# Kernel optimization log

Measured on AMD Instinct MI355X. Metric: run time of the kernel, lower is better.

Reference implementation:

```python
import jax, jax.numpy as jnp
import numpy as np

D = 128            # actual_dim
DM = 2 * D         # d_model = 256
DI = 2 * DM        # support-encoder inner dim = 512
H = 2 * DM         # LSTMCell hidden = 512
NUM_SYMBOLS = 200000
KNN_K = 10
PROCESS_STEPS = 4
BQ, BS, NN = 4096, 128, 64


def setup_inputs() -> dict:
    key = jax.random.key(0)
    ks = jax.random.split(key, 20)
    ri = lambda k, shape, hi: jax.random.randint(k, shape, 0, hi)
    rn = lambda k, shape, s=0.05: jax.random.normal(k, shape, jnp.float32) * s
    emb = rn(ks[0], (NUM_SYMBOLS + 1, D), 0.1).at[NUM_SYMBOLS].set(0.0)  # padding row
    return {
        "query": ri(ks[1], (BQ, 2), NUM_SYMBOLS),
        "support": ri(ks[2], (BS, 2), NUM_SYMBOLS),
        "q_l_conn": ri(ks[3], (BQ, NN, 2), NUM_SYMBOLS),
        "q_l_deg": ri(ks[4], (BQ,), NN),
        "q_r_conn": ri(ks[5], (BQ, NN, 2), NUM_SYMBOLS),
        "q_r_deg": ri(ks[6], (BQ,), NN),
        "s_l_conn": ri(ks[7], (BS, NN, 2), NUM_SYMBOLS),
        "s_l_deg": ri(ks[8], (BS,), NN),
        "s_r_conn": ri(ks[9], (BS, NN, 2), NUM_SYMBOLS),
        "s_r_deg": ri(ks[10], (BS,), NN),
        "emb": emb,
        "gcn_W": rn(ks[11], (D, 2 * D)),
        "gcn_wb": jnp.zeros((D,), jnp.float32),
        "gcn_b": jnp.zeros((D,), jnp.float32),
        "se_w1": rn(ks[12], (DI, DM)),
        "se_b1": jnp.zeros((DI,), jnp.float32),
        "se_w2": rn(ks[13], (DM, DI)),
        "se_b2": jnp.zeros((DM,), jnp.float32),
        "ln_g": jnp.ones((DM,), jnp.float32),
        "ln_b": jnp.zeros((DM,), jnp.float32),
        "W_ih": rn(ks[14], (4 * H, DM)),
        "W_hh": rn(ks[15], (4 * H, H)),
        "b_ih": jnp.zeros((4 * H,), jnp.float32),
        "b_hh": jnp.zeros((4 * H,), jnp.float32),
    }


def _cos(a, b, eps=1e-8):
    num = jnp.sum(a * b, -1)
    den = jnp.maximum(jnp.linalg.norm(a, axis=-1), eps) * jnp.maximum(jnp.linalg.norm(b, axis=-1), eps)
    return num / den


def _neighbor_encoder(emb, gcn_W, gcn_wb, gcn_b, conn, ent_ids):
    rel = emb[conn[..., 0]]                     # [B,N,D]
    ent = emb[conn[..., 1]]                     # [B,N,D]
    center = emb[ent_ids][:, None, :]           # [B,1,D]
    sim = _cos(center, ent)                     # [B,N]
    _, idx = jax.lax.top_k(sim, KNN_K)          # [B,K]
    rel_k = jnp.take_along_axis(rel, idx[..., None], axis=1)
    ent_k = jnp.take_along_axis(ent, idx[..., None], axis=1)
    cat = jnp.concatenate([rel_k, ent_k], -1)   # [B,K,2D]
    h = jnp.einsum('bkf,df->bkd', cat, gcn_W) + gcn_wb + gcn_b
    return jnp.tanh(h.mean(axis=1))             # [B,D]


def _support_encoder(x, w1, b1, w2, b2, g, b):
    # residual FFN + LayerNorm (GMatching SupportEncoder), dropout off (eval)
    out = jax.nn.relu(x @ w1.T + b1) @ w2.T + b2
    y = out + x
    mu = y.mean(-1, keepdims=True)
    var = ((y - mu) ** 2).mean(-1, keepdims=True)
    return (y - mu) / jnp.sqrt(var + 1e-5) * g + b


def _query_encoder(support, query, W_ih, W_hh, b_ih, b_hh):
    # GMatching attentive LSTM process block. support: [1,DM], query: [B,DM]
    B = query.shape[0]
    h_r = jnp.zeros((B, H), query.dtype)
    c = jnp.zeros((B, H), query.dtype)
    h = query
    for _ in range(PROCESS_STEPS):
        gates = query @ W_ih.T + b_ih + h_r @ W_hh.T + b_hh
        i, f, g_, o = jnp.split(gates, 4, axis=-1)  # torch LSTMCell gate order
        c = jax.nn.sigmoid(f) * c + jax.nn.sigmoid(i) * jnp.tanh(g_)
        h_new = jax.nn.sigmoid(o) * jnp.tanh(c)     # [B,H]
        h = query + h_new[:, :DM]                   # [B,DM]
        attn = jax.nn.softmax(h @ support.T, axis=1)  # [B,1]
        r = attn @ support                          # [B,DM]
        h_r = jnp.concatenate([h, r], axis=1)       # [B,H]
    return h


def reference(query, support, q_l_conn, q_l_deg, q_r_conn, q_r_deg,
              s_l_conn, s_l_deg, s_r_conn, s_r_deg,
              emb, gcn_W, gcn_wb, gcn_b,
              se_w1, se_b1, se_w2, se_b2, ln_g, ln_b,
              W_ih, W_hh, b_ih, b_hh):
    ne = lambda conn, ids: _neighbor_encoder(emb, gcn_W, gcn_wb, gcn_b, conn, ids)
    q_nb = jnp.concatenate([ne(q_l_conn, query[:, 0]), ne(q_r_conn, query[:, 1])], -1)    # [BQ,DM]
    s_nb = jnp.concatenate([ne(s_l_conn, support[:, 0]), ne(s_r_conn, support[:, 1])], -1)  # [BS,DM]
    se = lambda x: _support_encoder(x, se_w1, se_b1, se_w2, se_b2, ln_g, ln_b)
    support_g = se(s_nb).mean(axis=0, keepdims=True)  # [1,DM]
    query_g = se(q_nb)                                # [BQ,DM]
    qf = _query_encoder(support_g, query_g, W_ih, W_hh, b_ih, b_hh)
    l2 = lambda x: x / jnp.maximum(jnp.linalg.norm(x, axis=-1, keepdims=True), 1e-12)
    return (l2(qf) @ l2(support_g).T).squeeze(-1)     # [BQ]
```

## Files before the change

kernel.cpp:

```cpp
#include <hip/hip_runtime.h>
#include <hip/hip_bf16.h>

#define D   128
#define DM  256
#define DI  512
#define HH  512
#define KNN 10
#define NN  64
#define BQ  4096
#define BS  128
#define BM2 (BQ + BS)
#define G2  1024
#define GK  256
#define NSYM 200000
#define NEB (BQ * 2 + BS * 2)
#define BKT 64
#define LDP (BKT + 8)

__device__ __forceinline__ float sigmoidf_(float x) {
    return 1.f / (1.f + __expf(-x));
}
__device__ __forceinline__ float tanh_fast(float x) {
    x = fminf(fmaxf(x, -20.f), 20.f);
    float e = __expf(2.f * x);
    return (e - 1.f) / (e + 1.f);
}
__device__ __forceinline__ ushort f2bf(float x) {
    union { float f; unsigned u; } v; v.f = x;
    unsigned r = (v.u + 0x7fffu + ((v.u >> 16) & 1u)) >> 16;
    return (ushort)r;
}

typedef __bf16  bf16x8  __attribute__((ext_vector_type(8)));
typedef float   floatx4 __attribute__((ext_vector_type(4)));

__global__ __launch_bounds__(256) void ne_prep_kernel(
    const int* __restrict__ q_l, const int* __restrict__ q_r,
    const int* __restrict__ q_ids,
    const int* __restrict__ s_l, const int* __restrict__ s_r,
    const int* __restrict__ s_ids,
    const float* __restrict__ emb,
    float* __restrict__ catm_out,
    const float* __restrict__ W_ih, const float* __restrict__ W_hh,
    const float* __restrict__ b_ih, const float* __restrict__ b_hh,
    const float* __restrict__ se_w1, const float* __restrict__ se_w2,
    ushort* __restrict__ wih_bf, ushort* __restrict__ whh_bf,
    float* __restrict__ bsumP, ushort* __restrict__ w1_bf,
    ushort* __restrict__ w2_bf)
{
    int bid = blockIdx.x;
    int tid = threadIdx.x;

    if (bid >= NEB) {
        int pb = bid - NEB;
        if (pb < G2) {
            int n = pb;
            int bn = n >> 7, r = n & 127;
            int half = (r >> 6) & 1, j = (r >> 4) & 3, l = r & 15;
            int u = bn * 32 + half * 16 + l;
            int oldrow = j * 512 + u;
            wih_bf[n * 256 + tid] = f2bf(W_ih[(size_t)oldrow * DM + tid]);
            whh_bf[n * 256 + tid] = f2bf(W_hh[(size_t)oldrow * HH + tid]);
            if (tid == 0) bsumP[n] = b_ih[oldrow] + b_hh[oldrow];
        } else {
            int idx = (pb - G2) * 256 + tid;
            w1_bf[idx] = f2bf(se_w1[idx]);
            w2_bf[idx] = f2bf(se_w2[idx]);
        }
        return;
    }

    const int *conn_l, *conn_r, *ids;
    int row;
    if (bid < BQ * 2) { conn_l = q_l; conn_r = q_r; ids = q_ids; row = bid >> 1; }
    else { conn_l = s_l; conn_r = s_r; ids = s_ids; row = (bid - BQ * 2) >> 1; }
    int side = bid & 1;
    const int* conn = (side ? conn_r : conn_l) + (size_t)row * NN * 2;
    int cid = ids[row * 2 + side];

    __shared__ int   connb[NN * 2];
    __shared__ float sim[NN];
    __shared__ int   selr[KNN], sele[KNN];

    int wave = tid >> 6, lane = tid & 63;
    int grp = lane >> 4, l16 = lane & 15;

    if (tid < NN * 2) connb[tid] = conn[tid];
    const float* cp = &emb[(size_t)cid * D + l16 * 8];
    float4 c4a = *(const float4*)cp;
    float4 c4b = *(const float4*)(cp + 4);
    float cs = c4a.x * c4a.x + c4a.y * c4a.y + c4a.z * c4a.z + c4a.w * c4a.w
             + c4b.x * c4b.x + c4b.y * c4b.y + c4b.z * c4b.z + c4b.w * c4b.w;
    #pragma unroll
    for (int off = 8; off; off >>= 1) cs += __shfl_xor(cs, off);
    float cnorm = fmaxf(sqrtf(cs), 1e-8f);
    __syncthreads();

    float4 ea[4], eb[4];
    #pragma unroll
    for (int b = 0; b < 4; b++) {
        int j = wave * 16 + b * 4 + grp;
        int eid = connb[j * 2 + 1];
        const float* ep = &emb[(size_t)eid * D + l16 * 8];
        ea[b] = *(const float4*)ep;
        eb[b] = *(const float4*)(ep + 4);
    }
    #pragma unroll
    for (int b = 0; b < 4; b++) {
        int j = wave * 16 + b * 4 + grp;
        float dot = c4a.x * ea[b].x + c4a.y * ea[b].y + c4a.z * ea[b].z + c4a.w * ea[b].w
                  + c4b.x * eb[b].x + c4b.y * eb[b].y + c4b.z * eb[b].z + c4b.w * eb[b].w;
        float ee  = ea[b].x * ea[b].x + ea[b].y * ea[b].y + ea[b].z * ea[b].z + ea[b].w * ea[b].w
                  + eb[b].x * eb[b].x + eb[b].y * eb[b].y + eb[b].z * eb[b].z + eb[b].w * eb[b].w;
        #pragma unroll
        for (int off = 8; off; off >>= 1) {
            dot += __shfl_xor(dot, off);
            ee  += __shfl_xor(ee, off);
        }
        if (l16 == 0) sim[j] = dot / (cnorm * fmaxf(sqrtf(ee), 1e-8f));
    }
    __syncthreads();

    if (wave == 0) {
        float s = sim[lane];
        int id = lane;
        for (int k = 0; k < KNN; k++) {
            float bs = s; int bi = id;
            #pragma unroll
            for (int off = 32; off; off >>= 1) {
                float os = __shfl_xor(bs, off);
                int   oi = __shfl_xor(bi, off);
                if (os > bs || (os == bs && oi < bi)) { bs = os; bi = oi; }
            }
            if (lane == 0) { selr[k] = connb[bi * 2]; sele[k] = connb[bi * 2 + 1]; }
            if (id == bi) s = -__builtin_inff();
        }
    }
    __syncthreads();

    float acc = 0.f;
    if (tid < D) {
        #pragma unroll
        for (int k = 0; k < KNN; k++) acc += emb[(size_t)selr[k] * D + tid];
    } else {
        int d = tid - D;
        #pragma unroll
        for (int k = 0; k < KNN; k++) acc += emb[(size_t)sele[k] * D + d];
    }
    catm_out[(size_t)bid * DM + tid] = acc * (1.f / KNN);
}

#define GR 16
__global__ __launch_bounds__(256) void gcn_kernel(
    const float* __restrict__ catm, const float* __restrict__ gcn_W,
    const float* __restrict__ gcn_wb, const float* __restrict__ gcn_b,
    float* __restrict__ out, ushort* __restrict__ out_bf)
{
    __shared__ float cs[GR][DM];
    __shared__ float pp[GR][DM];
    int tid = threadIdx.x;
    int m0 = blockIdx.x * GR;
    #pragma unroll
    for (int t = 0; t < 4; t++) {
        int chunk = tid + 256 * t;
        int r = chunk >> 6, c4 = chunk & 63;
        *(float4*)&cs[r][c4 * 4] = *(const float4*)&catm[(size_t)(m0 + r) * DM + c4 * 4];
    }
    __syncthreads();

    int d = tid & 127, half = tid >> 7;
    float a[GR];
    #pragma unroll
    for (int r = 0; r < GR; r++) a[r] = 0.f;
    const float4* W4 = (const float4*)(gcn_W + (size_t)d * DM + half * D);
    for (int f4 = 0; f4 < D / 4; ++f4) {
        float4 w = W4[f4];
        #pragma unroll
        for (int r = 0; r < GR; r++) {
            const float* c = &cs[r][half * D + f4 * 4];
            a[r] += w.x * c[0] + w.y * c[1] + w.z * c[2] + w.w * c[3];
        }
    }
    #pragma unroll
    for (int r = 0; r < GR; r++) pp[r][tid] = a[r];
    __syncthreads();
    if (tid < D) {
        #pragma unroll
        for (int r = 0; r < GR; r++) {
            float h = pp[r][tid] + pp[r][tid + D] + gcn_wb[tid] + gcn_b[tid];
            float th = tanh_fast(h);
            out[(size_t)(m0 + r) * D + tid] = th;
            out_bf[(size_t)(m0 + r) * D + tid] = f2bf(th);
        }
    }
}

#define GEMM64_VARS()                                                         \
    __shared__ __align__(16) ushort As[64][LDP];                              \
    __shared__ __align__(16) ushort Bs[128][LDP];                             \
    int tid = threadIdx.x;                                                    \
    int wave = tid >> 6, lane = tid & 63;                                     \
    int quad = lane >> 4, l16 = lane & 15;                                    \
    int wm = (wave >> 1) * 32, wn = (wave & 1) * 64;

#define GEMM64_CORE(AP, BP, KDIM)                                             \
    floatx4 acc[2][4];                                                        \
    _Pragma("unroll")                                                         \
    for (int i = 0; i < 2; i++)                                               \
        _Pragma("unroll")                                                     \
        for (int j = 0; j < 4; j++) acc[i][j] = (floatx4){0.f, 0.f, 0.f, 0.f};\
    for (int k0 = 0; k0 < (KDIM); k0 += BKT) {                                \
        __syncthreads();                                                      \
        _Pragma("unroll")                                                     \
        for (int t = 0; t < 2; t++) {                                         \
            int ch = t * 256 + tid;                                           \
            int r = ch >> 3, c8 = (ch & 7) * 8;                               \
            *(uint4*)&As[r][c8] = *(const uint4*)&(AP)[(size_t)(bm * 64 + r) * (KDIM) + k0 + c8]; \
        }                                                                     \
        _Pragma("unroll")                                                     \
        for (int t = 0; t < 4; t++) {                                         \
            int ch = t * 256 + tid;                                           \
            int r = ch >> 3, c8 = (ch & 7) * 8;                               \
            *(uint4*)&Bs[r][c8] = *(const uint4*)&(BP)[(size_t)(bn * 128 + r) * (KDIM) + k0 + c8]; \
        }                                                                     \
        __syncthreads();                                                      \
        _Pragma("unroll")                                                     \
        for (int kk = 0; kk < BKT; kk += 32) {                                \
            bf16x8 af[2], bv[4];                                              \
            _Pragma("unroll")                                                 \
            for (int i = 0; i < 2; i++)                                       \
                af[i] = *(const bf16x8*)&As[wm + i * 16 + l16][kk + quad * 8];\
            _Pragma("unroll")                                                 \
            for (int j = 0; j < 4; j++)                                       \
                bv[j] = *(const bf16x8*)&Bs[wn + j * 16 + l16][kk + quad * 8];\
            _Pragma("unroll")                                                 \
            for (int i = 0; i < 2; i++)                                       \
                _Pragma("unroll")                                             \
                for (int j = 0; j < 4; j++)                                   \
                    acc[i][j] = __builtin_amdgcn_mfma_f32_16x16x32_bf16(      \
                        af[i], bv[j], acc[i][j], 0, 0, 0);                    \
        }                                                                     \
    }

__global__ __launch_bounds__(256) void se_gemm1_kernel(
    const ushort* __restrict__ A, const ushort* __restrict__ B,
    const float* __restrict__ b1, ushort* __restrict__ Cbf)
{
    GEMM64_VARS();
    int bm = blockIdx.x, bn = blockIdx.y;
    GEMM64_CORE(A, B, DM);
    #pragma unroll
    for (int i = 0; i < 2; i++) {
        #pragma unroll
        for (int j = 0; j < 4; j++) {
            int row = bm * 64 + wm + i * 16 + quad * 4;
            int col = bn * 128 + wn + j * 16 + l16;
            float bb = b1[col];
            #pragma unroll
            for (int rr = 0; rr < 4; rr++)
                Cbf[(size_t)(row + rr) * DI + col] = f2bf(fmaxf(acc[i][j][rr] + bb, 0.f));
        }
    }
}

__global__ __launch_bounds__(256) void se_gemm2_kernel(
    const ushort* __restrict__ A, const ushort* __restrict__ B,
    const float* __restrict__ b2, const float* __restrict__ xres,
    float* __restrict__ C)
{
    GEMM64_VARS();
    int bm = blockIdx.x, bn = blockIdx.y;
    GEMM64_CORE(A, B, DI);
    #pragma unroll
    for (int i = 0; i < 2; i++) {
        #pragma unroll
        for (int j = 0; j < 4; j++) {
            int row = bm * 64 + wm + i * 16 + quad * 4;
            int col = bn * 128 + wn + j * 16 + l16;
            float bb = b2[col];
            #pragma unroll
            for (int rr = 0; rr < 4; rr++)
                C[(size_t)(row + rr) * DM + col] =
                    acc[i][j][rr] + bb + xres[(size_t)(row + rr) * DM + col];
        }
    }
}

#define LN_ROWS 8
__global__ __launch_bounds__(256) void ln_kernel(
    const float* __restrict__ ys, const float* __restrict__ g,
    const float* __restrict__ b, float* __restrict__ outf,
    ushort* __restrict__ outbf)
{
    int tid = threadIdx.x;
    int wave = tid >> 6, lane = tid & 63;
    int r0 = blockIdx.x * LN_ROWS;
    for (int rr = 0; rr < 2; ++rr) {
        int r = r0 + wave * 2 + rr;
        float vals[4];
        float s = 0.f;
        #pragma unroll
        for (int e = 0; e < 4; e++) {
            vals[e] = ys[(size_t)r * DM + e * 64 + lane];
            s += vals[e];
        }
        #pragma unroll
        for (int off = 32; off; off >>= 1) s += __shfl_xor(s, off);
        float mu = s * (1.f / DM);
        float v = 0.f;
        #pragma unroll
        for (int e = 0; e < 4; e++) { float dd = vals[e] - mu; v += dd * dd; }
        #pragma unroll
        for (int off = 32; off; off >>= 1) v += __shfl_xor(v, off);
        float rstd = rsqrtf(v * (1.f / DM) + 1e-5f);
        #pragma unroll
        for (int e = 0; e < 4; e++) {
            int dd = e * 64 + lane;
            float ov = (vals[e] - mu) * rstd * g[dd] + b[dd];
            outf[(size_t)r * DM + dd] = ov;
            outbf[(size_t)r * DM + dd] = f2bf(ov);
        }
    }
}

__global__ __launch_bounds__(256) void lstm_gemm0_sgw_kernel(
    const ushort* __restrict__ A, const ushort* __restrict__ B,
    const float* __restrict__ bsumP, const float* __restrict__ lnf,
    float* __restrict__ P0f, float* __restrict__ Cf, ushort* __restrict__ h_out,
    const float* __restrict__ W_hh, const float* __restrict__ b_ih,
    const float* __restrict__ b_hh, float* __restrict__ sg,
    float* __restrict__ gaddP)
{
    if (blockIdx.x >= 512) {
        __shared__ float s[DM];
        int tid = threadIdx.x;
        int sb = blockIdx.x - 512;
        float a = 0.f;
        for (int r = 0; r < BS; r++) a += lnf[(size_t)(BQ + r) * DM + tid];
        a *= (1.f / BS);
        s[tid] = a;
        if (sb == 0) sg[tid] = a;
        __syncthreads();

        int idx = sb * 256 + tid;
        int g = idx >> 8, u = idx & 255;
        int oldrow = g * 512 + u;
        const float4* w4 = (const float4*)(W_hh + (size_t)oldrow * HH + DM);
        float acc = 0.f;
        for (int f4 = 0; f4 < DM / 4; ++f4) {
            float4 w = w4[f4];
            acc += w.x * s[f4 * 4] + w.y * s[f4 * 4 + 1] + w.z * s[f4 * 4 + 2] + w.w * s[f4 * 4 + 3];
        }
        float bs = b_ih[oldrow] + b_hh[oldrow];
        int n = (u >> 5) * 128 + ((u >> 4) & 1) * 64 + g * 16 + (u & 15);
        gaddP[n] = bs + acc;
        return;
    }

    GEMM64_VARS();
    int bm = blockIdx.x >> 3, bn = blockIdx.x & 7;
    GEMM64_CORE(A, B, GK);
    int u = bn * 32 + (wn ? 16 : 0) + l16;
    size_t tile = (size_t)bm * 8 + bn;
    float b4[4];
    #pragma unroll
    for (int j = 0; j < 4; j++) b4[j] = bsumP[bn * 128 + wn + j * 16 + l16];
    #pragma unroll
    for (int i = 0; i < 2; i++) {
        int row = bm * 64 + wm + i * 16 + quad * 4;
        #pragma unroll
        for (int j = 0; j < 4; j++)
            *(floatx4*)&P0f[((tile * 8 + i * 4 + j) * 256 + tid) * 4] = acc[i][j];
        floatx4 cv4;
        #pragma unroll
        for (int rr = 0; rr < 4; rr++) {
            float iv = acc[i][0][rr] + b4[0];
            float gv = acc[i][2][rr] + b4[2];
            float ov = acc[i][3][rr] + b4[3];
            float cv = sigmoidf_(iv) * tanh_fast(gv);
            cv4[rr] = cv;
            float h = lnf[(size_t)(row + rr) * DM + u] + sigmoidf_(ov) * tanh_fast(cv);
            h_out[(size_t)(row + rr) * DM + u] = f2bf(h);
        }
        *(floatx4*)&Cf[((tile * 2 + i) * 256 + tid) * 4] = cv4;
    }
}

__global__ __launch_bounds__(256) void lstm_step_kernel(
    const ushort* __restrict__ A, const ushort* __restrict__ B,
    const float* __restrict__ P0f, const float* __restrict__ gaddP,
    const float* __restrict__ lnf, float* __restrict__ Cf,
    ushort* __restrict__ h_out, float* __restrict__ hf_out, int last)
{
    GEMM64_VARS();
    int bm = blockIdx.x, bn = blockIdx.y;
    GEMM64_CORE(A, B, GK);
    int u = bn * 32 + (wn ? 16 : 0) + l16;
    size_t tile = (size_t)bm * 8 + bn;
    float g4[4];
    #pragma unroll
    for (int j = 0; j < 4; j++) g4[j] = gaddP[bn * 128 + wn + j * 16 + l16];
    #pragma unroll
    for (int i = 0; i < 2; i++) {
        int row = bm * 64 + wm + i * 16 + quad * 4;
        floatx4 p0[4];
        #pragma unroll
        for (int j = 0; j < 4; j++)
            p0[j] = *(const floatx4*)&P0f[((tile * 8 + i * 4 + j) * 256 + tid) * 4];
        floatx4 cprev = *(const floatx4*)&Cf[((tile * 2 + i) * 256 + tid) * 4];
        floatx4 cnew;
        #pragma unroll
        for (int rr = 0; rr < 4; rr++) {
            float iv = acc[i][0][rr] + p0[0][rr] + g4[0];
            float fv = acc[i][1][rr] + p0[1][rr] + g4[1];
            float gv = acc[i][2][rr] + p0[2][rr] + g4[2];
            float ov = acc[i][3][rr] + p0[3][rr] + g4[3];
            float cv = sigmoidf_(fv) * cprev[rr] + sigmoidf_(iv) * tanh_fast(gv);
            cnew[rr] = cv;
            float h = lnf[(size_t)(row + rr) * DM + u] + sigmoidf_(ov) * tanh_fast(cv);
            if (last) hf_out[(size_t)(row + rr) * DM + u] = h;
            else      h_out[(size_t)(row + rr) * DM + u] = f2bf(h);
        }
        *(floatx4*)&Cf[((tile * 2 + i) * 256 + tid) * 4] = cnew;
    }
}

__global__ __launch_bounds__(256) void final_kernel(
    const float* __restrict__ h_ws, const float* __restrict__ sg,
    float* __restrict__ outp)
{
    __shared__ float sgs[DM];
    int tid = threadIdx.x;
    sgs[tid] = sg[tid];
    __syncthreads();
    int wave = tid >> 6, lane = tid & 63;
    float sn = 0.f;
    #pragma unroll
    for (int e = 0; e < 4; e++) { float v = sgs[e * 64 + lane]; sn += v * v; }
    #pragma unroll
    for (int off = 32; off; off >>= 1) sn += __shfl_xor(sn, off);
    float sgnorm = fmaxf(sqrtf(sn), 1e-12f);

    int row = blockIdx.x * 4 + wave;
    const float* h = h_ws + (size_t)row * DM;
    float dot = 0.f, hn = 0.f;
    #pragma unroll
    for (int e = 0; e < 4; e++) {
        float hv = h[e * 64 + lane];
        dot += hv * sgs[e * 64 + lane];
        hn += hv * hv;
    }
    #pragma unroll
    for (int off = 32; off; off >>= 1) { dot += __shfl_xor(dot, off); hn += __shfl_xor(hn, off); }
    if (lane == 0) outp[row] = dot / (fmaxf(sqrtf(hn), 1e-12f) * sgnorm);
}

extern "C" void kernel_launch(void* const* d_in, const int* in_sizes, int n_in,
                              void* d_out, int out_size, void* d_ws, size_t ws_size,
                              hipStream_t stream)
{
    const int* query    = (const int*)d_in[0];
    const int* support  = (const int*)d_in[1];
    const int* q_l_conn = (const int*)d_in[2];
    const int* q_r_conn = (const int*)d_in[4];
    const int* s_l_conn = (const int*)d_in[6];
    const int* s_r_conn = (const int*)d_in[8];
    const float* emb    = (const float*)d_in[10];
    const float* gcn_W  = (const float*)d_in[11];
    const float* gcn_wb = (const float*)d_in[12];
    const float* gcn_b  = (const float*)d_in[13];
    const float* se_w1  = (const float*)d_in[14];
    const float* se_b1  = (const float*)d_in[15];
    const float* se_w2  = (const float*)d_in[16];
    const float* se_b2  = (const float*)d_in[17];
    const float* ln_g   = (const float*)d_in[18];
    const float* ln_b   = (const float*)d_in[19];
    const float* W_ih   = (const float*)d_in[20];
    const float* W_hh   = (const float*)d_in[21];
    const float* b_ih   = (const float*)d_in[22];
    const float* b_hh   = (const float*)d_in[23];
    float* out = (float*)d_out;

    char* wsb = (char*)d_ws;
    float*  xf     = (float*)wsb;  wsb += (size_t)BM2 * DM * 4;
    ushort* xb     = (ushort*)wsb; wsb += (size_t)BM2 * DM * 2;
    ushort* t1_bf  = (ushort*)wsb; wsb += (size_t)BM2 * DI * 2;
    float*  ys     = (float*)wsb;  wsb += (size_t)BM2 * DM * 4;
    float*  ln_f   = (float*)wsb;  wsb += (size_t)BM2 * DM * 4;
    ushort* ln_bf  = (ushort*)wsb; wsb += (size_t)BM2 * DM * 2;
    float*  sg     = (float*)wsb;  wsb += DM * 4;
    float*  bsumP  = (float*)wsb;  wsb += G2 * 4;
    float*  gaddP  = (float*)wsb;  wsb += G2 * 4;
    ushort* wih_bf = (ushort*)wsb; wsb += (size_t)G2 * DM * 2;
    ushort* whh_bf = (ushort*)wsb; wsb += (size_t)G2 * DM * 2;
    ushort* w1_bf  = (ushort*)wsb; wsb += (size_t)DI * DM * 2;
    ushort* w2_bf  = (ushort*)wsb; wsb += (size_t)DM * DI * 2;
    float*  P0f    = (float*)wsb;  wsb += (size_t)BQ * G2 * 4;
    float*  Cf     = (float*)wsb;  wsb += (size_t)BQ * DM * 4;
    ushort* h_bfA  = (ushort*)wsb; wsb += (size_t)BQ * DM * 2;
    ushort* h_bfB  = (ushort*)wsb; wsb += (size_t)BQ * DM * 2;
    float*  h_f    = (float*)wsb;  wsb += (size_t)BQ * DM * 4;

    float* catm = P0f;

    ne_prep_kernel<<<NEB + G2 + 512, 256, 0, stream>>>(
        q_l_conn, q_r_conn, query, s_l_conn, s_r_conn, support,
        emb, catm,
        W_ih, W_hh, b_ih, b_hh, se_w1, se_w2,
        wih_bf, whh_bf, bsumP, w1_bf, w2_bf);
    gcn_kernel<<<(BM2 * 2) / GR, 256, 0, stream>>>(catm, gcn_W, gcn_wb, gcn_b,
                                                   xf, xb);
    { dim3 g1(BM2 / 64, DI / 128);
      se_gemm1_kernel<<<g1, 256, 0, stream>>>(xb, w1_bf, se_b1, t1_bf); }
    { dim3 g2(BM2 / 64, DM / 128);
      se_gemm2_kernel<<<g2, 256, 0, stream>>>(t1_bf, w2_bf, se_b2, xf, ys); }
    ln_kernel<<<BM2 / LN_ROWS, 256, 0, stream>>>(ys, ln_g, ln_b, ln_f, ln_bf);

    lstm_gemm0_sgw_kernel<<<516, 256, 0, stream>>>(
        ln_bf, wih_bf, bsumP, ln_f, P0f, Cf, h_bfA,
        W_hh, b_ih, b_hh, sg, gaddP);

    dim3 ggrid(BQ / 64, G2 / 128);
    lstm_step_kernel<<<ggrid, 256, 0, stream>>>(h_bfA, whh_bf, P0f, gaddP, ln_f,
                                                Cf, h_bfB, h_f, 0);
    lstm_step_kernel<<<ggrid, 256, 0, stream>>>(h_bfB, whh_bf, P0f, gaddP, ln_f,
                                                Cf, h_bfA, h_f, 0);
    lstm_step_kernel<<<ggrid, 256, 0, stream>>>(h_bfA, whh_bf, P0f, gaddP, ln_f,
                                                Cf, h_bfB, h_f, 1);
    final_kernel<<<BQ / 4, 256, 0, stream>>>(h_f, sg, out);
}
```

Baseline: 335.6 us.

## Fuse GCN, support-encoder GEMMs and LayerNorm into one kernel

Replaces four separate kernels (GCN projection, two support-encoder GEMMs, LayerNorm) with one mid_kernel. Each block processes 16 output rows and keeps intermediates (tanh output, ReLU hidden, residual sum) in swizzled shared memory instead of global buffers. This removes the global round-trips for xf, xb, t1 and ys and three launches. In exchange each block streams the full w1/w2 weights straight from global memory without LDS staging, uses 64KB of shared memory, and runs only 264 blocks, so occupancy is lower.

```diff
diff --git a/kernel.cpp b/kernel.cpp
--- a/kernel.cpp
+++ b/kernel.cpp
@@ -150,47 +150,154 @@
     catm_out[(size_t)bid * DM + tid] = acc * (1.f / KNN);
 }
 
-#define GR 16
-__global__ __launch_bounds__(256) void gcn_kernel(
-    const float* __restrict__ catm, const float* __restrict__ gcn_W,
-    const float* __restrict__ gcn_wb, const float* __restrict__ gcn_b,
-    float* __restrict__ out, ushort* __restrict__ out_bf)
+__global__ __launch_bounds__(256) void mid_kernel(
+    const float* __restrict__ catm,
+    const float* __restrict__ gcn_W, const float* __restrict__ gcn_wb,
+    const float* __restrict__ gcn_b,
+    const ushort* __restrict__ w1, const float* __restrict__ b1,
+    const ushort* __restrict__ w2, const float* __restrict__ b2,
+    const float* __restrict__ ln_g, const float* __restrict__ ln_b,
+    float* __restrict__ outf, ushort* __restrict__ outbf)
 {
-    __shared__ float cs[GR][DM];
-    __shared__ float pp[GR][DM];
+    __shared__ __align__(16) char smem[65536];
+    float*  catm_s = (float*)smem;
+    float*  xs     = (float*)smem;
+    ushort* xb_s   = (ushort*)(smem + 16384);
+    float*  pp     = (float*)(smem + 32768);
+    ushort* t1s    = (ushort*)(smem + 32768);
+    float*  ys_s   = (float*)(smem + 49152);
+
     int tid = threadIdx.x;
-    int m0 = blockIdx.x * GR;
-    #pragma unroll
-    for (int t = 0; t < 4; t++) {
-        int chunk = tid + 256 * t;
-        int r = chunk >> 6, c4 = chunk & 63;
-        *(float4*)&cs[r][c4 * 4] = *(const float4*)&catm[(size_t)(m0 + r) * DM + c4 * 4];
-    }
-    __syncthreads();
-
-    int d = tid & 127, half = tid >> 7;
-    float a[GR];
-    #pragma unroll
-    for (int r = 0; r < GR; r++) a[r] = 0.f;
-    const float4* W4 = (const float4*)(gcn_W + (size_t)d * DM + half * D);
-    for (int f4 = 0; f4 < D / 4; ++f4) {
-        float4 w = W4[f4];
-        #pragma unroll
-        for (int r = 0; r < GR; r++) {
-            const float* c = &cs[r][half * D + f4 * 4];
-            a[r] += w.x * c[0] + w.y * c[1] + w.z * c[2] + w.w * c[3];
-        }
-    }
-    #pragma unroll
-    for (int r = 0; r < GR; r++) pp[r][tid] = a[r];
-    __syncthreads();
+    int bm = blockIdx.x;
+    int wave = tid >> 6, lane = tid & 63;
+    int quad = lane >> 4, l16 = lane & 15;
+
+    #pragma unroll
+    for (int t = 0; t < 8; t++) {
+        int ch = t * 256 + tid;
+        int r = ch >> 6, c4 = ch & 63;
+        *(float4*)&catm_s[r * 256 + c4 * 4] =
+            *(const float4*)&catm[(size_t)(bm * 32 + r) * DM + c4 * 4];
+    }
+    __syncthreads();
+
+    {
+        int d = tid & 127, half = tid >> 7;
+        float a[32];
+        #pragma unroll
+        for (int r = 0; r < 32; r++) a[r] = 0.f;
+        const float4* W4 = (const float4*)(gcn_W + (size_t)d * DM + half * D);
+        for (int f4 = 0; f4 < D / 4; ++f4) {
+            float4 w = W4[f4];
+            #pragma unroll
+            for (int r = 0; r < 32; r++) {
+                const float* c = &catm_s[r * 256 + half * D + f4 * 4];
+                a[r] += w.x * c[0] + w.y * c[1] + w.z * c[2] + w.w * c[3];
+            }
+        }
+        #pragma unroll
+        for (int r = 0; r < 32; r++) pp[r * 256 + tid] = a[r];
+    }
+    __syncthreads();
+
     if (tid < D) {
         #pragma unroll
-        for (int r = 0; r < GR; r++) {
-            float h = pp[r][tid] + pp[r][tid + D] + gcn_wb[tid] + gcn_b[tid];
+        for (int r = 0; r < 32; r++) {
+            float h = pp[r * 256 + tid] + pp[r * 256 + tid + D] + gcn_wb[tid] + gcn_b[tid];
             float th = tanh_fast(h);
-            out[(size_t)(m0 + r) * D + tid] = th;
-            out_bf[(size_t)(m0 + r) * D + tid] = f2bf(th);
+            xs[r * 128 + tid] = th;
+            int c16 = tid >> 3, e = tid & 7;
+            xb_s[r * 128 + (((c16 ^ ((r >> 1) & 15)) << 3) + e)] = f2bf(th);
+        }
+    }
+    __syncthreads();
+
+    {
+        floatx4 acc[8];
+        #pragma unroll
+        for (int j = 0; j < 8; j++) acc[j] = (floatx4){0.f, 0.f, 0.f, 0.f};
+        #pragma unroll
+        for (int kk = 0; kk < DM; kk += 32) {
+            int c = (kk >> 3) + quad;
+            int r = 2 * l16 + (c >= 16);
+            int c15 = c & 15;
+            bf16x8 af = *(const bf16x8*)&xb_s[r * 128 + ((c15 ^ l16) << 3)];
+            #pragma unroll
+            for (int j = 0; j < 8; j++) {
+                int cr = wave * 128 + j * 16 + l16;
+                bf16x8 bv = *(const bf16x8*)&w1[(size_t)cr * DM + kk + quad * 8];
+                acc[j] = __builtin_amdgcn_mfma_f32_16x16x32_bf16(af, bv, acc[j], 0, 0, 0);
+            }
+        }
+        #pragma unroll
+        for (int j = 0; j < 8; j++) {
+            int col = wave * 128 + j * 16 + l16;
+            float bb = b1[col];
+            #pragma unroll
+            for (int rr = 0; rr < 4; rr++) {
+                int m = quad * 4 + rr;
+                float v = fmaxf(acc[j][rr] + bb, 0.f);
+                int cc = col >> 3, e = col & 7;
+                t1s[m * 512 + (((cc ^ (m & 15)) << 3) + e)] = f2bf(v);
+            }
+        }
+    }
+    __syncthreads();
+
+    {
+        floatx4 acc[4];
+        #pragma unroll
+        for (int j = 0; j < 4; j++) acc[j] = (floatx4){0.f, 0.f, 0.f, 0.f};
+        #pragma unroll
+        for (int kk = 0; kk < DI; kk += 32) {
+            int c = (kk >> 3) + quad;
+            bf16x8 af = *(const bf16x8*)&t1s[l16 * 512 + ((c ^ l16) << 3)];
+            #pragma unroll
+            for (int j = 0; j < 4; j++) {
+                int cr = wave * 64 + j * 16 + l16;
+                bf16x8 bv = *(const bf16x8*)&w2[(size_t)cr * DI + kk + quad * 8];
+                acc[j] = __builtin_amdgcn_mfma_f32_16x16x32_bf16(af, bv, acc[j], 0, 0, 0);
+            }
+        }
+        #pragma unroll
+        for (int j = 0; j < 4; j++) {
+            int col = wave * 64 + j * 16 + l16;
+            float bb = b2[col];
+            #pragma unroll
+            for (int rr = 0; rr < 4; rr++) {
+                int m = quad * 4 + rr;
+                ys_s[m * 256 + col] = acc[j][rr] + bb + xs[m * 256 + col];
+            }
+        }
+    }
+    __syncthreads();
+
+    #pragma unroll
+    for (int rr2 = 0; rr2 < 4; rr2++) {
+        int m = wave * 4 + rr2;
+        int rg = bm * 16 + m;
+        float vals[4];
+        float s = 0.f;
+        #pragma unroll
+        for (int e = 0; e < 4; e++) {
+            vals[e] = ys_s[m * 256 + e * 64 + lane];
+            s += vals[e];
+        }
+        #pragma unroll
+        for (int off = 32; off; off >>= 1) s += __shfl_xor(s, off);
+        float mu = s * (1.f / DM);
+        float v = 0.f;
+        #pragma unroll
+        for (int e = 0; e < 4; e++) { float dd = vals[e] - mu; v += dd * dd; }
+        #pragma unroll
+        for (int off = 32; off; off >>= 1) v += __shfl_xor(v, off);
+        float rstd = rsqrtf(v * (1.f / DM) + 1e-5f);
+        #pragma unroll
+        for (int e = 0; e < 4; e++) {
+            int dd = e * 64 + lane;
+            float ov = (vals[e] - mu) * rstd * ln_g[dd] + ln_b[dd];
+            outf[(size_t)rg * DM + dd] = ov;
+            outbf[(size_t)rg * DM + dd] = f2bf(ov);
         }
     }
 }
@@ -242,87 +349,6 @@
         }                                                                     \
     }
 
-__global__ __launch_bounds__(256) void se_gemm1_kernel(
-    const ushort* __restrict__ A, const ushort* __restrict__ B,
-    const float* __restrict__ b1, ushort* __restrict__ Cbf)
-{
-    GEMM64_VARS();
-    int bm = blockIdx.x, bn = blockIdx.y;
-    GEMM64_CORE(A, B, DM);
-    #pragma unroll
-    for (int i = 0; i < 2; i++) {
-        #pragma unroll
-        for (int j = 0; j < 4; j++) {
-            int row = bm * 64 + wm + i * 16 + quad * 4;
-            int col = bn * 128 + wn + j * 16 + l16;
-            float bb = b1[col];
-            #pragma unroll
-            for (int rr = 0; rr < 4; rr++)
-                Cbf[(size_t)(row + rr) * DI + col] = f2bf(fmaxf(acc[i][j][rr] + bb, 0.f));
-        }
-    }
-}
-
-__global__ __launch_bounds__(256) void se_gemm2_kernel(
-    const ushort* __restrict__ A, const ushort* __restrict__ B,
-    const float* __restrict__ b2, const float* __restrict__ xres,
-    float* __restrict__ C)
-{
-    GEMM64_VARS();
-    int bm = blockIdx.x, bn = blockIdx.y;
-    GEMM64_CORE(A, B, DI);
-    #pragma unroll
-    for (int i = 0; i < 2; i++) {
-        #pragma unroll
-        for (int j = 0; j < 4; j++) {
-            int row = bm * 64 + wm + i * 16 + quad * 4;
-            int col = bn * 128 + wn + j * 16 + l16;
-            float bb = b2[col];
-            #pragma unroll
-            for (int rr = 0; rr < 4; rr++)
-                C[(size_t)(row + rr) * DM + col] =
-                    acc[i][j][rr] + bb + xres[(size_t)(row + rr) * DM + col];
-        }
-    }
-}
-
-#define LN_ROWS 8
-__global__ __launch_bounds__(256) void ln_kernel(
-    const float* __restrict__ ys, const float* __restrict__ g,
-    const float* __restrict__ b, float* __restrict__ outf,
-    ushort* __restrict__ outbf)
-{
-    int tid = threadIdx.x;
-    int wave = tid >> 6, lane = tid & 63;
-    int r0 = blockIdx.x * LN_ROWS;
-    for (int rr = 0; rr < 2; ++rr) {
-        int r = r0 + wave * 2 + rr;
-        float vals[4];
-        float s = 0.f;
-        #pragma unroll
-        for (int e = 0; e < 4; e++) {
-            vals[e] = ys[(size_t)r * DM + e * 64 + lane];
-            s += vals[e];
-        }
-        #pragma unroll
-        for (int off = 32; off; off >>= 1) s += __shfl_xor(s, off);
-        float mu = s * (1.f / DM);
-        float v = 0.f;
-        #pragma unroll
-        for (int e = 0; e < 4; e++) { float dd = vals[e] - mu; v += dd * dd; }
-        #pragma unroll
-        for (int off = 32; off; off >>= 1) v += __shfl_xor(v, off);
-        float rstd = rsqrtf(v * (1.f / DM) + 1e-5f);
-        #pragma unroll
-        for (int e = 0; e < 4; e++) {
-            int dd = e * 64 + lane;
-            float ov = (vals[e] - mu) * rstd * g[dd] + b[dd];
-            outf[(size_t)r * DM + dd] = ov;
-            outbf[(size_t)r * DM + dd] = f2bf(ov);
-        }
-    }
-}
-
 __global__ __launch_bounds__(256) void lstm_gemm0_sgw_kernel(
     const ushort* __restrict__ A, const ushort* __restrict__ B,
     const float* __restrict__ bsumP, const float* __restrict__ lnf,
@@ -482,10 +508,6 @@
     float* out = (float*)d_out;
 
     char* wsb = (char*)d_ws;
-    float*  xf     = (float*)wsb;  wsb += (size_t)BM2 * DM * 4;
-    ushort* xb     = (ushort*)wsb; wsb += (size_t)BM2 * DM * 2;
-    ushort* t1_bf  = (ushort*)wsb; wsb += (size_t)BM2 * DI * 2;
-    float*  ys     = (float*)wsb;  wsb += (size_t)BM2 * DM * 4;
     float*  ln_f   = (float*)wsb;  wsb += (size_t)BM2 * DM * 4;
     ushort* ln_bf  = (ushort*)wsb; wsb += (size_t)BM2 * DM * 2;
     float*  sg     = (float*)wsb;  wsb += DM * 4;
@@ -508,13 +530,11 @@
         emb, catm,
         W_ih, W_hh, b_ih, b_hh, se_w1, se_w2,
         wih_bf, whh_bf, bsumP, w1_bf, w2_bf);
-    gcn_kernel<<<(BM2 * 2) / GR, 256, 0, stream>>>(catm, gcn_W, gcn_wb, gcn_b,
-                                                   xf, xb);
-    { dim3 g1(BM2 / 64, DI / 128);
-      se_gemm1_kernel<<<g1, 256, 0, stream>>>(xb, w1_bf, se_b1, t1_bf); }
-    { dim3 g2(BM2 / 64, DM / 128);
-      se_gemm2_kernel<<<g2, 256, 0, stream>>>(t1_bf, w2_bf, se_b2, xf, ys); }
-    ln_kernel<<<BM2 / LN_ROWS, 256, 0, stream>>>(ys, ln_g, ln_b, ln_f, ln_bf);
+
+    mid_kernel<<<BM2 / 16, 256, 0, stream>>>(
+        catm, gcn_W, gcn_wb, gcn_b,
+        w1_bf, se_b1, w2_bf, se_b2, ln_g, ln_b,
+        ln_f, ln_bf);
 
     lstm_gemm0_sgw_kernel<<<516, 256, 0, stream>>>(
         ln_bf, wih_bf, bsumP, ln_f, P0f, Cf, h_bfA,
```

Result: slower. 342.9 us (+2.2%).

## Recompute input projection in each LSTM step instead of storing P0 gates

Applied to the files above, without the earlier changes.

Interleaves W_ih and the first half of W_hh into one combined bf16 weight matrix and has each LSTM step run a K=512 GEMM over [ln_bf, h] rather than reading a precomputed fp32 input-projection tensor P0f (BQ x 1024 floats). This removes writing P0f once and reading it three times, trading that memory traffic for double the MFMA work per step. The catm buffer gets its own workspace region since P0f no longer exists.

```diff
diff --git a/kernel.cpp b/kernel.cpp
--- a/kernel.cpp
+++ b/kernel.cpp
@@ -44,7 +44,7 @@
     const float* __restrict__ W_ih, const float* __restrict__ W_hh,
     const float* __restrict__ b_ih, const float* __restrict__ b_hh,
     const float* __restrict__ se_w1, const float* __restrict__ se_w2,
-    ushort* __restrict__ wih_bf, ushort* __restrict__ whh_bf,
+    ushort* __restrict__ wcomb,
     float* __restrict__ bsumP, ushort* __restrict__ w1_bf,
     ushort* __restrict__ w2_bf)
 {
@@ -59,8 +59,8 @@
             int half = (r >> 6) & 1, j = (r >> 4) & 3, l = r & 15;
             int u = bn * 32 + half * 16 + l;
             int oldrow = j * 512 + u;
-            wih_bf[n * 256 + tid] = f2bf(W_ih[(size_t)oldrow * DM + tid]);
-            whh_bf[n * 256 + tid] = f2bf(W_hh[(size_t)oldrow * HH + tid]);
+            wcomb[(size_t)n * 512 + tid]       = f2bf(W_ih[(size_t)oldrow * DM + tid]);
+            wcomb[(size_t)n * 512 + 256 + tid] = f2bf(W_hh[(size_t)oldrow * HH + tid]);
             if (tid == 0) bsumP[n] = b_ih[oldrow] + b_hh[oldrow];
         } else {
             int idx = (pb - G2) * 256 + tid;
@@ -324,9 +324,9 @@
 }
 
 __global__ __launch_bounds__(256) void lstm_gemm0_sgw_kernel(
-    const ushort* __restrict__ A, const ushort* __restrict__ B,
+    const ushort* __restrict__ A, const ushort* __restrict__ wcomb,
     const float* __restrict__ bsumP, const float* __restrict__ lnf,
-    float* __restrict__ P0f, float* __restrict__ Cf, ushort* __restrict__ h_out,
+    float* __restrict__ Cf, ushort* __restrict__ h_out,
     const float* __restrict__ W_hh, const float* __restrict__ b_ih,
     const float* __restrict__ b_hh, float* __restrict__ sg,
     float* __restrict__ gaddP)
@@ -359,7 +359,43 @@
 
     GEMM64_VARS();
     int bm = blockIdx.x >> 3, bn = blockIdx.x & 7;
-    GEMM64_CORE(A, B, GK);
+    floatx4 acc[2][4];
+    #pragma unroll
+    for (int i = 0; i < 2; i++)
+        #pragma unroll
+        for (int j = 0; j < 4; j++) acc[i][j] = (floatx4){0.f, 0.f, 0.f, 0.f};
+    for (int k0 = 0; k0 < GK; k0 += BKT) {
+        __syncthreads();
+        #pragma unroll
+        for (int t = 0; t < 2; t++) {
+            int ch = t * 256 + tid;
+            int r = ch >> 3, c8 = (ch & 7) * 8;
+            *(uint4*)&As[r][c8] = *(const uint4*)&A[(size_t)(bm * 64 + r) * GK + k0 + c8];
+        }
+        #pragma unroll
+        for (int t = 0; t < 4; t++) {
+            int ch = t * 256 + tid;
+            int r = ch >> 3, c8 = (ch & 7) * 8;
+            *(uint4*)&Bs[r][c8] = *(const uint4*)&wcomb[(size_t)(bn * 128 + r) * 512 + k0 + c8];
+        }
+        __syncthreads();
+        #pragma unroll
+        for (int kk = 0; kk < BKT; kk += 32) {
+            bf16x8 af[2], bv[4];
+            #pragma unroll
+            for (int i = 0; i < 2; i++)
+                af[i] = *(const bf16x8*)&As[wm + i * 16 + l16][kk + quad * 8];
+            #pragma unroll
+            for (int j = 0; j < 4; j++)
+                bv[j] = *(const bf16x8*)&Bs[wn + j * 16 + l16][kk + quad * 8];
+            #pragma unroll
+            for (int i = 0; i < 2; i++)
+                #pragma unroll
+                for (int j = 0; j < 4; j++)
+                    acc[i][j] = __builtin_amdgcn_mfma_f32_16x16x32_bf16(
+                        af[i], bv[j], acc[i][j], 0, 0, 0);
+        }
+    }
     int u = bn * 32 + (wn ? 16 : 0) + l16;
     size_t tile = (size_t)bm * 8 + bn;
     float b4[4];
@@ -368,9 +404,6 @@
     #pragma unroll
     for (int i = 0; i < 2; i++) {
         int row = bm * 64 + wm + i * 16 + quad * 4;
-        #pragma unroll
-        for (int j = 0; j < 4; j++)
-            *(floatx4*)&P0f[((tile * 8 + i * 4 + j) * 256 + tid) * 4] = acc[i][j];
         floatx4 cv4;
         #pragma unroll
         for (int rr = 0; rr < 4; rr++) {
@@ -387,14 +420,51 @@
 }
 
 __global__ __launch_bounds__(256) void lstm_step_kernel(
-    const ushort* __restrict__ A, const ushort* __restrict__ B,
-    const float* __restrict__ P0f, const float* __restrict__ gaddP,
+    const ushort* __restrict__ lnbf, const ushort* __restrict__ hin,
+    const ushort* __restrict__ wcomb, const float* __restrict__ gaddP,
     const float* __restrict__ lnf, float* __restrict__ Cf,
     ushort* __restrict__ h_out, float* __restrict__ hf_out, int last)
 {
     GEMM64_VARS();
     int bm = blockIdx.x, bn = blockIdx.y;
-    GEMM64_CORE(A, B, GK);
+    floatx4 acc[2][4];
+    #pragma unroll
+    for (int i = 0; i < 2; i++)
+        #pragma unroll
+        for (int j = 0; j < 4; j++) acc[i][j] = (floatx4){0.f, 0.f, 0.f, 0.f};
+    for (int k0 = 0; k0 < 512; k0 += BKT) {
+        const ushort* Abase = (k0 < 256) ? (lnbf + k0) : (hin + (k0 - 256));
+        __syncthreads();
+        #pragma unroll
+        for (int t = 0; t < 2; t++) {
+            int ch = t * 256 + tid;
+            int r = ch >> 3, c8 = (ch & 7) * 8;
+            *(uint4*)&As[r][c8] = *(const uint4*)&Abase[(size_t)(bm * 64 + r) * 256 + c8];
+        }
+        #pragma unroll
+        for (int t = 0; t < 4; t++) {
+            int ch = t * 256 + tid;
+            int r = ch >> 3, c8 = (ch & 7) * 8;
+            *(uint4*)&Bs[r][c8] = *(const uint4*)&wcomb[(size_t)(bn * 128 + r) * 512 + k0 + c8];
+        }
+        __syncthreads();
+        #pragma unroll
+        for (int kk = 0; kk < BKT; kk += 32) {
+            bf16x8 af[2], bv[4];
+            #pragma unroll
+            for (int i = 0; i < 2; i++)
+                af[i] = *(const bf16x8*)&As[wm + i * 16 + l16][kk + quad * 8];
+            #pragma unroll
+            for (int j = 0; j < 4; j++)
+                bv[j] = *(const bf16x8*)&Bs[wn + j * 16 + l16][kk + quad * 8];
+            #pragma unroll
+            for (int i = 0; i < 2; i++)
+                #pragma unroll
+                for (int j = 0; j < 4; j++)
+                    acc[i][j] = __builtin_amdgcn_mfma_f32_16x16x32_bf16(
+                        af[i], bv[j], acc[i][j], 0, 0, 0);
+        }
+    }
     int u = bn * 32 + (wn ? 16 : 0) + l16;
     size_t tile = (size_t)bm * 8 + bn;
     float g4[4];
@@ -403,18 +473,14 @@
     #pragma unroll
     for (int i = 0; i < 2; i++) {
         int row = bm * 64 + wm + i * 16 + quad * 4;
-        floatx4 p0[4];
-        #pragma unroll
-        for (int j = 0; j < 4; j++)
-            p0[j] = *(const floatx4*)&P0f[((tile * 8 + i * 4 + j) * 256 + tid) * 4];
         floatx4 cprev = *(const floatx4*)&Cf[((tile * 2 + i) * 256 + tid) * 4];
         floatx4 cnew;
         #pragma unroll
         for (int rr = 0; rr < 4; rr++) {
-            float iv = acc[i][0][rr] + p0[0][rr] + g4[0];
-            float fv = acc[i][1][rr] + p0[1][rr] + g4[1];
-            float gv = acc[i][2][rr] + p0[2][rr] + g4[2];
-            float ov = acc[i][3][rr] + p0[3][rr] + g4[3];
+            float iv = acc[i][0][rr] + g4[0];
+            float fv = acc[i][1][rr] + g4[1];
+            float gv = acc[i][2][rr] + g4[2];
+            float ov = acc[i][3][rr] + g4[3];
             float cv = sigmoidf_(fv) * cprev[rr] + sigmoidf_(iv) * tanh_fast(gv);
             cnew[rr] = cv;
             float h = lnf[(size_t)(row + rr) * DM + u] + sigmoidf_(ov) * tanh_fast(cv);
@@ -491,23 +557,20 @@
     float*  sg     = (float*)wsb;  wsb += DM * 4;
     float*  bsumP  = (float*)wsb;  wsb += G2 * 4;
     float*  gaddP  = (float*)wsb;  wsb += G2 * 4;
-    ushort* wih_bf = (ushort*)wsb; wsb += (size_t)G2 * DM * 2;
-    ushort* whh_bf = (ushort*)wsb; wsb += (size_t)G2 * DM * 2;
+    ushort* wcomb  = (ushort*)wsb; wsb += (size_t)G2 * 512 * 2;
     ushort* w1_bf  = (ushort*)wsb; wsb += (size_t)DI * DM * 2;
     ushort* w2_bf  = (ushort*)wsb; wsb += (size_t)DM * DI * 2;
-    float*  P0f    = (float*)wsb;  wsb += (size_t)BQ * G2 * 4;
+    float*  catm   = (float*)wsb;  wsb += (size_t)NEB * DM * 4;
     float*  Cf     = (float*)wsb;  wsb += (size_t)BQ * DM * 4;
     ushort* h_bfA  = (ushort*)wsb; wsb += (size_t)BQ * DM * 2;
     ushort* h_bfB  = (ushort*)wsb; wsb += (size_t)BQ * DM * 2;
     float*  h_f    = (float*)wsb;  wsb += (size_t)BQ * DM * 4;
 
-    float* catm = P0f;
-
     ne_prep_kernel<<<NEB + G2 + 512, 256, 0, stream>>>(
         q_l_conn, q_r_conn, query, s_l_conn, s_r_conn, support,
         emb, catm,
         W_ih, W_hh, b_ih, b_hh, se_w1, se_w2,
-        wih_bf, whh_bf, bsumP, w1_bf, w2_bf);
+        wcomb, bsumP, w1_bf, w2_bf);
     gcn_kernel<<<(BM2 * 2) / GR, 256, 0, stream>>>(catm, gcn_W, gcn_wb, gcn_b,
                                                    xf, xb);
     { dim3 g1(BM2 / 64, DI / 128);
@@ -517,15 +580,15 @@
     ln_kernel<<<BM2 / LN_ROWS, 256, 0, stream>>>(ys, ln_g, ln_b, ln_f, ln_bf);
 
     lstm_gemm0_sgw_kernel<<<516, 256, 0, stream>>>(
-        ln_bf, wih_bf, bsumP, ln_f, P0f, Cf, h_bfA,
+        ln_bf, wcomb, bsumP, ln_f, Cf, h_bfA,
         W_hh, b_ih, b_hh, sg, gaddP);
 
     dim3 ggrid(BQ / 64, G2 / 128);
-    lstm_step_kernel<<<ggrid, 256, 0, stream>>>(h_bfA, whh_bf, P0f, gaddP, ln_f,
+    lstm_step_kernel<<<ggrid, 256, 0, stream>>>(ln_bf, h_bfA, wcomb, gaddP, ln_f,
                                                 Cf, h_bfB, h_f, 0);
-    lstm_step_kernel<<<ggrid, 256, 0, stream>>>(h_bfB, whh_bf, P0f, gaddP, ln_f,
+    lstm_step_kernel<<<ggrid, 256, 0, stream>>>(ln_bf, h_bfB, wcomb, gaddP, ln_f,
                                                 Cf, h_bfA, h_f, 0);
-    lstm_step_kernel<<<ggrid, 256, 0, stream>>>(h_bfA, whh_bf, P0f, gaddP, ln_f,
+    lstm_step_kernel<<<ggrid, 256, 0, stream>>>(ln_bf, h_bfA, wcomb, gaddP, ln_f,
                                                 Cf, h_bfB, h_f, 1);
     final_kernel<<<BQ / 4, 256, 0, stream>>>(h_f, sg, out);
 }
```

Measured after the change: 338.7 us, median of 2. About the same (+0.9%).
